# Kernel tuning notes

Hardware: AMD Instinct MI355X
Metric: run time of the kernel (lower is better)

Reference implementation:

```python
import jax, jax.numpy as jnp
import numpy as np

BIG_Z = 1e6  # sentinel used for background depth when finding the nearest mesh


def setup_inputs() -> dict:
    key = jax.random.key(0)
    ks = jax.random.split(key, 6)
    N, H, W, K = 8, 512, 512, 1      # n_mesh, image H, image W, faces_per_pixel
    F, V, C = 20000, 10002, 32       # faces, verts, feature channels
    zbuf = jax.random.normal(ks[0], (N, H, W, K), jnp.float32)  # ~half negative = background
    pix_to_face = jax.random.randint(ks[1], (N, H, W, K), -1, F)  # -1 = no face
    b = jax.random.uniform(ks[2], (N, H, W, K, 3), jnp.float32) + 1e-3
    bary_coords = b / jnp.sum(b, axis=-1, keepdims=True)
    dists = jax.random.uniform(ks[3], (N, H, W, K), jnp.float32)
    face_memory = jax.random.normal(ks[4], (F, 3, C), jnp.float32)
    packed_faces = jax.random.randint(ks[5], (F, 3), 0, V)
    return {
        "zbuf": zbuf,
        "pix_to_face": pix_to_face,
        "bary_coords": bary_coords,
        "dists": dists,
        "face_memory": face_memory,
        "packed_faces": packed_faces,
        "num_verts": V,
        "mask_duplicate": 0,
    }


def reference(zbuf, pix_to_face, bary_coords, dists, face_memory, packed_faces,
              num_verts, mask_duplicate):
    N = zbuf.shape[0]
    Fn = face_memory.shape[0]

    # per-object mask BEFORE occlusion masking (zbuf[..., 0] >= 0)
    per_obj_mask = zbuf[..., 0] >= 0  # [N,H,W]

    # _mask_occluded_object: pixels covered by >1 mesh
    covered = (zbuf > -1)
    dup = jnp.sum(covered.astype(jnp.float32), axis=0, keepdims=True) > 1  # [1,H,W,K]
    dup = jnp.broadcast_to(dup, zbuf.shape)  # [N,H,W,K]
    if not mask_duplicate:
        # keep the nearest (min-z) mesh at duplicate pixels
        tmp = jnp.where(zbuf < 0, BIG_Z, zbuf)
        min_idx = jnp.argmin(tmp, axis=0)  # [H,W,K]
        mesh_ids = jnp.arange(N).reshape(N, 1, 1, 1)
        dup = dup & (mesh_ids != min_idx[None])

    # mask occluded fragments to -1 (matches in-place boolean writes)
    p = jnp.where(dup, -1, pix_to_face)
    bc = jnp.where(dup[..., None], -1.0, bary_coords)
    d = jnp.where(dup, -1.0, dists)
    zb = jnp.where(dup, -1.0, zbuf)

    # interpolate_face_attributes: gather [N,H,W,K,3,C] then bary-weighted sum,
    # zeroing pixels with pix_to_face < 0
    valid = p >= 0
    safe = jnp.where(valid, p, 0)
    attrs = face_memory[safe]  # [N,H,W,K,3,C]
    out = jnp.einsum('nhwki,nhwkic->nhwkc', bc, attrs)
    out = out * valid[..., None].astype(out.dtype)
    out_map = out[:, :, :, 0, :]               # squeeze K dim -> [N,H,W,C]
    out_map = jnp.transpose(out_map, (0, 3, 1, 2))  # -> [N,C,H,W]

    # vertex visibility: unique visible faces -> their vertices get 1.0
    face_hit = jnp.zeros((Fn,), jnp.float32).at[safe.ravel()].add(
        valid.ravel().astype(jnp.float32))
    face_vis = (face_hit > 0).astype(jnp.float32)  # [F]
    vv = jnp.zeros((num_verts,), jnp.float32).at[packed_faces.ravel()].add(
        jnp.broadcast_to(face_vis[:, None], (Fn, 3)).ravel())
    vertex_visibility_map = (vv > 0).astype(jnp.float32)

    # return out_map, visibility, per-object mask, and masked fragments (frags_clone)
    return out_map, vertex_visibility_map, per_obj_mask, zb, p, d, bc
```

## Files before the change

### kernel.cpp

```cpp
#include <hip/hip_runtime.h>

#define BIG_Z_F 1000000.0f
#define N_MESH 8

typedef float f4 __attribute__((ext_vector_type(4)));
typedef int   i4 __attribute__((ext_vector_type(4)));
typedef unsigned char uc4 __attribute__((ext_vector_type(4)));


__global__ __launch_bounds__(256) void raster_reduce(
    const f4* __restrict__ zbuf4,
    f4* __restrict__ maskO4,
    f4* __restrict__ zbO4,
    uc4* __restrict__ win4,
    int* __restrict__ faceflag,
    float* __restrict__ vv,
    const int* __restrict__ mdp,
    int HW4, int F, int V)
{
    const int q = blockIdx.x * blockDim.x + threadIdx.x;
    if (q >= HW4) return;

    if (q <= F) faceflag[q] = 0;
    if (q < V)  vv[q] = 0.0f;

    const int md = *mdp;

    float z[N_MESH][4];
    #pragma unroll
    for (int n = 0; n < N_MESH; ++n) {
        const f4 v = __builtin_nontemporal_load(&zbuf4[n * HW4 + q]);
        z[n][0] = v.x; z[n][1] = v.y; z[n][2] = v.z; z[n][3] = v.w;
    }

    bool dup0[4]; int bidx[4];
    #pragma unroll
    for (int j = 0; j < 4; ++j) {
        int count = 0; float best = __builtin_inff(); int bi = 0;
        #pragma unroll
        for (int n = 0; n < N_MESH; ++n) {
            const float zv = z[n][j];
            count += (zv > -1.0f) ? 1 : 0;
            const float t = (zv < 0.0f) ? BIG_Z_F : zv;
            if (t < best) { best = t; bi = n; }
        }
        dup0[j] = (count > 1);
        bidx[j] = bi;
    }

    #pragma unroll
    for (int n = 0; n < N_MESH; ++n) {
        f4 m, zb;
        #pragma unroll
        for (int j = 0; j < 4; ++j) {
            const bool dup = dup0[j] && ((md != 0) || (n != bidx[j]));
            m[j]  = (z[n][j] >= 0.0f) ? 1.0f : 0.0f;
            zb[j] = dup ? -1.0f : z[n][j];
        }
        __builtin_nontemporal_store(m,  &maskO4[n * HW4 + q]);
        __builtin_nontemporal_store(zb, &zbO4[n * HW4 + q]);
    }
    uc4 w;
    w.x = dup0[0] ? (unsigned char)bidx[0] : (unsigned char)0xFF;
    w.y = dup0[1] ? (unsigned char)bidx[1] : (unsigned char)0xFF;
    w.z = dup0[2] ? (unsigned char)bidx[2] : (unsigned char)0xFF;
    w.w = dup0[3] ? (unsigned char)bidx[3] : (unsigned char)0xFF;
    win4[q] = w;
}

__global__ __launch_bounds__(256) void raster_interp(
    const i4* __restrict__ p2f4,
    const f4* __restrict__ bary4,
    const f4* __restrict__ dists4,
    const float* __restrict__ fmem,
    const uc4* __restrict__ win4,
    const int* __restrict__ mdp,
    f4* __restrict__ out_map4,
    f4* __restrict__ pO4,
    f4* __restrict__ dO4,
    f4* __restrict__ bcO4,
    int* __restrict__ faceflag,
    int HW4, int C, int F)
{
    const int q = blockIdx.x * blockDim.x + threadIdx.x;
    if (q >= HW4) return;
    const int n    = blockIdx.y;
    const int idx4 = n * HW4 + q;
    const int md   = *mdp;

    const uc4 wv = win4[q];
    const unsigned char w[4] = { wv.x, wv.y, wv.z, wv.w };

    const i4 praw = __builtin_nontemporal_load(&p2f4[idx4]);
    const f4 drw  = __builtin_nontemporal_load(&dists4[idx4]);
    const f4 bv0  = __builtin_nontemporal_load(&bary4[idx4 * 3 + 0]);
    const f4 bv1  = __builtin_nontemporal_load(&bary4[idx4 * 3 + 1]);
    const f4 bv2  = __builtin_nontemporal_load(&bary4[idx4 * 3 + 2]);
    const int   pr[4] = { praw.x, praw.y, praw.z, praw.w };
    const float dr[4] = { drw.x, drw.y, drw.z, drw.w };
    const float br[4][3] = {
        { bv0.x, bv0.y, bv0.z },
        { bv0.w, bv1.x, bv1.y },
        { bv1.z, bv1.w, bv2.x },
        { bv2.y, bv2.z, bv2.w },
    };

    float bst[4][3];
    float bc[4][3];
    int   safe[4];
    f4 pOv, dOv;
    #pragma unroll
    for (int j = 0; j < 4; ++j) {
        const bool dup   = (w[j] != 0xFF) && ((md != 0) || (n != (int)w[j]));
        const int  p     = dup ? -1 : pr[j];
        const bool valid = (p >= 0);
        #pragma unroll
        for (int k = 0; k < 3; ++k) {
            bst[j][k] = dup ? -1.0f : br[j][k];
            bc[j][k]  = valid ? bst[j][k] : 0.0f;
        }
        safe[j] = valid ? p : 0;
        pOv[j]  = (float)p;
        dOv[j]  = dup ? -1.0f : dr[j];
        faceflag[valid ? p : F] = 1;
    }
    __builtin_nontemporal_store(pOv, &pO4[idx4]);
    __builtin_nontemporal_store(dOv, &dO4[idx4]);
    {
        f4 c0, c1, c2;
        c0.x = bst[0][0]; c0.y = bst[0][1]; c0.z = bst[0][2]; c0.w = bst[1][0];
        c1.x = bst[1][1]; c1.y = bst[1][2]; c1.z = bst[2][0]; c1.w = bst[2][1];
        c2.x = bst[2][2]; c2.y = bst[3][0]; c2.z = bst[3][1]; c2.w = bst[3][2];
        __builtin_nontemporal_store(c0, &bcO4[idx4 * 3 + 0]);
        __builtin_nontemporal_store(c1, &bcO4[idx4 * 3 + 1]);
        __builtin_nontemporal_store(c2, &bcO4[idx4 * 3 + 2]);
    }

    const float* ab[4];
    #pragma unroll
    for (int j = 0; j < 4; ++j)
        ab[j] = fmem + (size_t)safe[j] * 3 * C;

    #pragma unroll
    for (int c4 = 0; c4 < 32; c4 += 4) {
        f4 r[4];
        #pragma unroll
        for (int j = 0; j < 4; ++j) {
            const float* a = ab[j];
            const f4 a0 = *(const f4*)(a + c4);
            const f4 a1 = *(const f4*)(a + C + c4);
            const f4 a2 = *(const f4*)(a + 2 * C + c4);
            r[j] = bc[j][0] * a0 + bc[j][1] * a1 + bc[j][2] * a2;
        }
        #pragma unroll
        for (int k = 0; k < 4; ++k) {
            f4 o;
            o.x = r[0][k]; o.y = r[1][k]; o.z = r[2][k]; o.w = r[3][k];
            __builtin_nontemporal_store(o, &out_map4[(size_t)(n * C + c4 + k) * HW4 + q]);
        }
    }
}

__global__ __launch_bounds__(256) void vert_vis(
    const int* __restrict__ faceflag,
    const int* __restrict__ pfaces,
    float* __restrict__ vv,
    int F)
{
    const int f = blockIdx.x * blockDim.x + threadIdx.x;
    if (f >= F) return;
    if (faceflag[f]) {
        vv[pfaces[f * 3 + 0]] = 1.0f;
        vv[pfaces[f * 3 + 1]] = 1.0f;
        vv[pfaces[f * 3 + 2]] = 1.0f;
    }
}

extern "C" void kernel_launch(void* const* d_in, const int* in_sizes, int n_in,
                              void* d_out, int out_size, void* d_ws, size_t ws_size,
                              hipStream_t stream) {
    const float* zbuf   = (const float*)d_in[0];
    const int*   p2f    = (const int*)  d_in[1];
    const float* bary   = (const float*)d_in[2];
    const float* dists  = (const float*)d_in[3];
    const float* fmem   = (const float*)d_in[4];
    const int*   pfaces = (const int*)  d_in[5];
    const int*   mdp    = (const int*)  d_in[7];

    const long long P  = in_sizes[0];
    const int HW  = (int)(P / N_MESH);
    const int HW4 = HW / 4;
    const int F3  = in_sizes[5];
    const int F   = F3 / 3;
    const int C   = in_sizes[4] / F3;
    const int V   = (int)((long long)out_size - P * C - 7 * P);

    float* out     = (float*)d_out;
    float* out_map = out;
    float* vv      = out_map + P * C;
    float* maskO   = vv + V;
    float* zbO     = maskO + P;
    float* pO      = zbO + P;
    float* dO      = pO + P;
    float* bcO     = dO + P;

    int* faceflag = (int*)d_ws;
    uc4* win4     = (uc4*)(faceflag + F + 4);

    raster_reduce<<<dim3(HW4 / 256), dim3(256), 0, stream>>>(
        (const f4*)zbuf, (f4*)maskO, (f4*)zbO, win4, faceflag, vv, mdp,
        HW4, F, V);

    raster_interp<<<dim3(HW4 / 256, N_MESH), dim3(256), 0, stream>>>(
        (const i4*)p2f, (const f4*)bary, (const f4*)dists, fmem,
        (const uc4*)win4, mdp,
        (f4*)out_map, (f4*)pO, (f4*)dO, (f4*)bcO,
        faceflag, HW4, C, F);

    vert_vis<<<dim3((F + 255) / 256), dim3(256), 0, stream>>>(
        faceflag, pfaces, vv, F);
}
```

Measured before the change: 386.9 us.

## Fuse depth reduction and vertex visibility into the per-mesh interpolation kernel

Replaces the separate depth-reduce kernel with a per-mesh recomputation: each thread in the interp kernel reads all 8 mesh depths to find the duplicate count and nearest mesh, then writes its own mask and zbuf output. Vertex visibility is now set directly per valid pixel by scattering 1.0 into vv through packed_faces, which removes the faceflag workspace and the vert_vis kernel. A small kernel zeroes vv first. The trade-off is 8x redundant zbuf reads, mostly served from cache, and many more scattered vv stores (up to 3 per valid pixel) in place of one per face.

```diff
diff --git a/kernel.cpp b/kernel.cpp
--- a/kernel.cpp
+++ b/kernel.cpp
@@ -5,82 +5,31 @@
 
 typedef float f4 __attribute__((ext_vector_type(4)));
 typedef int   i4 __attribute__((ext_vector_type(4)));
-typedef unsigned char uc4 __attribute__((ext_vector_type(4)));
 
 
-__global__ __launch_bounds__(256) void raster_reduce(
-    const f4* __restrict__ zbuf4,
-    f4* __restrict__ maskO4,
-    f4* __restrict__ zbO4,
-    uc4* __restrict__ win4,
-    int* __restrict__ faceflag,
-    float* __restrict__ vv,
-    const int* __restrict__ mdp,
-    int HW4, int F, int V)
+__global__ __launch_bounds__(256) void zero_vv(
+    float* __restrict__ vv, int V)
 {
-    const int q = blockIdx.x * blockDim.x + threadIdx.x;
-    if (q >= HW4) return;
-
-    if (q <= F) faceflag[q] = 0;
-    if (q < V)  vv[q] = 0.0f;
-
-    const int md = *mdp;
-
-    float z[N_MESH][4];
-    #pragma unroll
-    for (int n = 0; n < N_MESH; ++n) {
-        const f4 v = __builtin_nontemporal_load(&zbuf4[n * HW4 + q]);
-        z[n][0] = v.x; z[n][1] = v.y; z[n][2] = v.z; z[n][3] = v.w;
-    }
-
-    bool dup0[4]; int bidx[4];
-    #pragma unroll
-    for (int j = 0; j < 4; ++j) {
-        int count = 0; float best = __builtin_inff(); int bi = 0;
-        #pragma unroll
-        for (int n = 0; n < N_MESH; ++n) {
-            const float zv = z[n][j];
-            count += (zv > -1.0f) ? 1 : 0;
-            const float t = (zv < 0.0f) ? BIG_Z_F : zv;
-            if (t < best) { best = t; bi = n; }
-        }
-        dup0[j] = (count > 1);
-        bidx[j] = bi;
-    }
-
-    #pragma unroll
-    for (int n = 0; n < N_MESH; ++n) {
-        f4 m, zb;
-        #pragma unroll
-        for (int j = 0; j < 4; ++j) {
-            const bool dup = dup0[j] && ((md != 0) || (n != bidx[j]));
-            m[j]  = (z[n][j] >= 0.0f) ? 1.0f : 0.0f;
-            zb[j] = dup ? -1.0f : z[n][j];
-        }
-        __builtin_nontemporal_store(m,  &maskO4[n * HW4 + q]);
-        __builtin_nontemporal_store(zb, &zbO4[n * HW4 + q]);
-    }
-    uc4 w;
-    w.x = dup0[0] ? (unsigned char)bidx[0] : (unsigned char)0xFF;
-    w.y = dup0[1] ? (unsigned char)bidx[1] : (unsigned char)0xFF;
-    w.z = dup0[2] ? (unsigned char)bidx[2] : (unsigned char)0xFF;
-    w.w = dup0[3] ? (unsigned char)bidx[3] : (unsigned char)0xFF;
-    win4[q] = w;
+    const int i = blockIdx.x * blockDim.x + threadIdx.x;
+    if (i < V) vv[i] = 0.0f;
 }
 
-__global__ __launch_bounds__(256) void raster_interp(
+__global__ __launch_bounds__(256) void raster_fused(
+    const f4* __restrict__ zbuf4,
     const i4* __restrict__ p2f4,
     const f4* __restrict__ bary4,
     const f4* __restrict__ dists4,
     const float* __restrict__ fmem,
-    const uc4* __restrict__ win4,
+    const int* __restrict__ pfaces,
     const int* __restrict__ mdp,
     f4* __restrict__ out_map4,
+    f4* __restrict__ maskO4,
+    f4* __restrict__ zbO4,
     f4* __restrict__ pO4,
     f4* __restrict__ dO4,
     f4* __restrict__ bcO4,
-    int* __restrict__ faceflag,
-    int HW4, int C, int F)
+    float* __restrict__ vv,
+    int HW4, int C)
 {
     const int q = blockIdx.x * blockDim.x + threadIdx.x;
     if (q >= HW4) return;
@@ -88,8 +37,37 @@
     const int idx4 = n * HW4 + q;
     const int md   = *mdp;
 
-    const uc4 wv = win4[q];
-    const unsigned char w[4] = { wv.x, wv.y, wv.z, wv.w };
+    int   cnt[4]  = { 0, 0, 0, 0 };
+    float best[4] = { __builtin_inff(), __builtin_inff(),
+                      __builtin_inff(), __builtin_inff() };
+    int   bi[4]   = { 0, 0, 0, 0 };
+    f4 zown;
+    #pragma unroll
+    for (int nn = 0; nn < N_MESH; ++nn) {
+        const f4 v = zbuf4[nn * HW4 + q];
+        if (nn == n) zown = v;
+        #pragma unroll
+        for (int j = 0; j < 4; ++j) {
+            const float zv = v[j];
+            cnt[j] += (zv > -1.0f) ? 1 : 0;
+            const float t = (zv < 0.0f) ? BIG_Z_F : zv;
+            if (t < best[j]) { best[j] = t; bi[j] = nn; }
+        }
+    }
+
+    bool dup[4];
+    {
+        f4 m, zb;
+        #pragma unroll
+        for (int j = 0; j < 4; ++j) {
+            const bool dup0 = (cnt[j] > 1);
+            dup[j] = dup0 && ((md != 0) || (n != bi[j]));
+            m[j]  = (zown[j] >= 0.0f) ? 1.0f : 0.0f;
+            zb[j] = dup[j] ? -1.0f : zown[j];
+        }
+        __builtin_nontemporal_store(m,  &maskO4[idx4]);
+        __builtin_nontemporal_store(zb, &zbO4[idx4]);
+    }
 
     const i4 praw = __builtin_nontemporal_load(&p2f4[idx4]);
     const f4 drw  = __builtin_nontemporal_load(&dists4[idx4]);
@@ -108,21 +86,21 @@
     float bst[4][3];
     float bc[4][3];
     int   safe[4];
+    bool  vld[4];
     f4 pOv, dOv;
     #pragma unroll
     for (int j = 0; j < 4; ++j) {
-        const bool dup   = (w[j] != 0xFF) && ((md != 0) || (n != (int)w[j]));
-        const int  p     = dup ? -1 : pr[j];
+        const int  p     = dup[j] ? -1 : pr[j];
         const bool valid = (p >= 0);
         #pragma unroll
         for (int k = 0; k < 3; ++k) {
-            bst[j][k] = dup ? -1.0f : br[j][k];
+            bst[j][k] = dup[j] ? -1.0f : br[j][k];
             bc[j][k]  = valid ? bst[j][k] : 0.0f;
         }
         safe[j] = valid ? p : 0;
+        vld[j]  = valid;
         pOv[j]  = (float)p;
-        dOv[j]  = dup ? -1.0f : dr[j];
-        faceflag[valid ? p : F] = 1;
+        dOv[j]  = dup[j] ? -1.0f : dr[j];
     }
     __builtin_nontemporal_store(pOv, &pO4[idx4]);
     __builtin_nontemporal_store(dOv, &dO4[idx4]);
@@ -134,6 +112,16 @@
         __builtin_nontemporal_store(c0, &bcO4[idx4 * 3 + 0]);
         __builtin_nontemporal_store(c1, &bcO4[idx4 * 3 + 1]);
         __builtin_nontemporal_store(c2, &bcO4[idx4 * 3 + 2]);
+    }
+
+    #pragma unroll
+    for (int j = 0; j < 4; ++j) {
+        if (vld[j]) {
+            const int b = safe[j] * 3;
+            vv[pfaces[b + 0]] = 1.0f;
+            vv[pfaces[b + 1]] = 1.0f;
+            vv[pfaces[b + 2]] = 1.0f;
+        }
     }
 
     const float* ab[4];
@@ -161,21 +149,6 @@
     }
 }
 
-__global__ __launch_bounds__(256) void vert_vis(
-    const int* __restrict__ faceflag,
-    const int* __restrict__ pfaces,
-    float* __restrict__ vv,
-    int F)
-{
-    const int f = blockIdx.x * blockDim.x + threadIdx.x;
-    if (f >= F) return;
-    if (faceflag[f]) {
-        vv[pfaces[f * 3 + 0]] = 1.0f;
-        vv[pfaces[f * 3 + 1]] = 1.0f;
-        vv[pfaces[f * 3 + 2]] = 1.0f;
-    }
-}
-
 extern "C" void kernel_launch(void* const* d_in, const int* in_sizes, int n_in,
                               void* d_out, int out_size, void* d_ws, size_t ws_size,
                               hipStream_t stream) {
@@ -191,7 +164,6 @@
     const int HW  = (int)(P / N_MESH);
     const int HW4 = HW / 4;
     const int F3  = in_sizes[5];
-    const int F   = F3 / 3;
     const int C   = in_sizes[4] / F3;
     const int V   = (int)((long long)out_size - P * C - 7 * P);
 
@@ -204,19 +176,11 @@
     float* dO      = pO + P;
     float* bcO     = dO + P;
 
-    int* faceflag = (int*)d_ws;
-    uc4* win4     = (uc4*)(faceflag + F + 4);
+    zero_vv<<<dim3((V + 255) / 256), dim3(256), 0, stream>>>(vv, V);
 
-    raster_reduce<<<dim3(HW4 / 256), dim3(256), 0, stream>>>(
-        (const f4*)zbuf, (f4*)maskO, (f4*)zbO, win4, faceflag, vv, mdp,
-        HW4, F, V);
-
-    raster_interp<<<dim3(HW4 / 256, N_MESH), dim3(256), 0, stream>>>(
-        (const i4*)p2f, (const f4*)bary, (const f4*)dists, fmem,
-        (const uc4*)win4, mdp,
-        (f4*)out_map, (f4*)pO, (f4*)dO, (f4*)bcO,
-        faceflag, HW4, C, F);
-
-    vert_vis<<<dim3((F + 255) / 256), dim3(256), 0, stream>>>(
-        faceflag, pfaces, vv, F);
+    raster_fused<<<dim3(HW4 / 256, N_MESH), dim3(256), 0, stream>>>(
+        (const f4*)zbuf, (const i4*)p2f, (const f4*)bary, (const f4*)dists,
+        fmem, pfaces, mdp,
+        (f4*)out_map, (f4*)maskO, (f4*)zbO, (f4*)pO, (f4*)dO, (f4*)bcO,
+        vv, HW4, C);
 }
```

Measured after the change: 395.4 us. +2.2%, slower.
